# Optimization experiments

Hardware: AMD Instinct MI355X
Metric: run time of the kernel (lower is better)

The kernel has to match this reference:

```python
import jax, jax.numpy as jnp
import numpy as np

D_MODEL = 512
D_STATE = 16
D_CONV = 4
EXPAND = 2
D_INNER = EXPAND * D_MODEL          # 1024
DT_RANK = (D_MODEL + 15) // 16      # 32
B, L = 32, 2048
EPS = 1e-12


def _ln(x, g, b):
    mu = jnp.mean(x, axis=-1, keepdims=True)
    var = jnp.mean(jnp.square(x - mu), axis=-1, keepdims=True)
    return (x - mu) * jax.lax.rsqrt(var + EPS) * g + b


def setup_inputs() -> dict:
    key = jax.random.key(0)
    ks = jax.random.split(key, 12)
    s = lambda fan: 1.0 / np.sqrt(fan)
    inp = {
        "input_tensor": jax.random.normal(ks[0], (B, L, D_MODEL), jnp.float32),
        # Mamba params
        "in_proj_w": jax.random.normal(ks[1], (2 * D_INNER, D_MODEL), jnp.float32) * s(D_MODEL),
        "conv_w": jax.random.normal(ks[2], (D_INNER, D_CONV), jnp.float32) * s(D_CONV),
        "conv_b": jnp.zeros((D_INNER,), jnp.float32),
        "x_proj_w": jax.random.normal(ks[3], (DT_RANK + 2 * D_STATE, D_INNER), jnp.float32) * s(D_INNER),
        "dt_proj_w": jax.random.normal(ks[4], (D_INNER, DT_RANK), jnp.float32) * s(DT_RANK),
        "dt_proj_b": jnp.full((D_INNER,), -4.0, jnp.float32),  # softplus(-4) ~ small dt
        "A_log": jnp.log(jnp.broadcast_to(jnp.arange(1, D_STATE + 1, dtype=jnp.float32), (D_INNER, D_STATE))),
        "D": jnp.ones((D_INNER,), jnp.float32),
        "out_proj_w": jax.random.normal(ks[5], (D_MODEL, D_INNER), jnp.float32) * s(D_INNER),
        # block params
        "ln1_g": jnp.ones((D_MODEL,), jnp.float32),
        "ln1_b": jnp.zeros((D_MODEL,), jnp.float32),
        "w1_w": jax.random.normal(ks[6], (4 * D_MODEL, D_MODEL), jnp.float32) * s(D_MODEL),
        "w1_b": jnp.zeros((4 * D_MODEL,), jnp.float32),
        "w2_w": jax.random.normal(ks[7], (D_MODEL, 4 * D_MODEL), jnp.float32) * s(4 * D_MODEL),
        "w2_b": jnp.zeros((D_MODEL,), jnp.float32),
        "ln2_g": jnp.ones((D_MODEL,), jnp.float32),
        "ln2_b": jnp.zeros((D_MODEL,), jnp.float32),
    }
    return inp


def _mamba(x, in_proj_w, conv_w, conv_b, x_proj_w, dt_proj_w, dt_proj_b, A_log, D, out_proj_w):
    # x: [B, L, d_model]
    xz = jnp.einsum("bld,ed->ble", x, in_proj_w)          # [B,L,2*d_inner]
    xi, z = jnp.split(xz, 2, axis=-1)                      # each [B,L,d_inner]

    # depthwise causal conv1d along L (d_conv taps)
    xpad = jnp.pad(xi, ((0, 0), (D_CONV - 1, 0), (0, 0)))
    conv = conv_b
    for k in range(D_CONV):
        conv = conv + xpad[:, k:k + L, :] * conv_w[:, k]
    u = jax.nn.silu(conv)                                  # [B,L,d_inner]

    # input-dependent dt, B, C
    x_dbl = jnp.einsum("bld,ed->ble", u, x_proj_w)         # [B,L,dt_rank+2N]
    dt, B_t, C_t = jnp.split(x_dbl, [DT_RANK, DT_RANK + D_STATE], axis=-1)
    delta = jax.nn.softplus(jnp.einsum("blr,dr->bld", dt, dt_proj_w) + dt_proj_b)  # [B,L,d_inner]

    A = -jnp.exp(A_log)                                    # [d_inner, N]

    def step(h, inp):
        u_t, d_t, Bt, Ct = inp                             # [B,d_in],[B,d_in],[B,N],[B,N]
        dA = jnp.exp(d_t[..., None] * A)                   # [B,d_in,N]
        h = h * dA + (d_t * u_t)[..., None] * Bt[:, None, :]
        y = jnp.sum(h * Ct[:, None, :], axis=-1)           # [B,d_in]
        return h, y

    h0 = jnp.zeros((B, D_INNER, D_STATE), u.dtype)
    xs = (jnp.swapaxes(u, 0, 1), jnp.swapaxes(delta, 0, 1),
          jnp.swapaxes(B_t, 0, 1), jnp.swapaxes(C_t, 0, 1))
    _, ys = jax.lax.scan(step, h0, xs)                     # [L,B,d_inner]
    y = jnp.swapaxes(ys, 0, 1) + u * D
    y = y * jax.nn.silu(z)
    return jnp.einsum("ble,de->bld", y, out_proj_w)        # [B,L,d_model]


def reference(input_tensor, in_proj_w, conv_w, conv_b, x_proj_w, dt_proj_w, dt_proj_b,
              A_log, D, out_proj_w, ln1_g, ln1_b, w1_w, w1_b, w2_w, w2_b, ln2_g, ln2_b):
    h = _mamba(input_tensor, in_proj_w, conv_w, conv_b, x_proj_w, dt_proj_w,
               dt_proj_b, A_log, D, out_proj_w)
    h = _ln(h + input_tensor, ln1_g, ln1_b)                # num_layers > 1 branch, dropout=0
    f = jax.nn.gelu(jnp.einsum("bld,fd->blf", h, w1_w) + w1_b, approximate=False)
    f = jnp.einsum("blf,df->bld", f, w2_w) + w2_b
    return _ln(f + h, ln2_g, ln2_b)
```

## Files before the change

### kernel.cpp

```cpp
#include <hip/hip_runtime.h>
#include <hip/hip_bf16.h>

#define DM 512
#define DI 1024
#define DC 4
#define DTR 32
#define NST 16
#define LSEQ 2048
#define NBATCH 32
#define NCH 32
#define CHL 64

typedef __attribute__((ext_vector_type(8))) short b16x8;
typedef __attribute__((ext_vector_type(4))) float fx4;
typedef __attribute__((ext_vector_type(4))) unsigned short u16x4;

__device__ __forceinline__ unsigned short f2bf(float f) {
    union { float f; unsigned u; } x; x.f = f;
    unsigned r = x.u + 0x7fffu + ((x.u >> 16) & 1u);
    return (unsigned short)(r >> 16);
}
__device__ __forceinline__ float bf2f(unsigned short u) {
    union { unsigned u; float f; } x; x.u = ((unsigned)u) << 16;
    return x.f;
}

__global__ __launch_bounds__(256) void cast_kernel(const float* __restrict__ src,
                                                   unsigned short* __restrict__ dst, int n4) {
    int i = blockIdx.x * 256 + threadIdx.x;
    if (i < n4) {
        fx4 v = *(const fx4*)&src[(size_t)i * 4];
        u16x4 o;
        #pragma unroll
        for (int j = 0; j < 4; j++) o[j] = f2bf(v[j]);
        *(u16x4*)&dst[(size_t)i * 4] = o;
    }
}

template <int BN, int BK, int EPI, bool HAS_BIAS>
__global__ __launch_bounds__(256, 3) void gemm_bf16(const unsigned short* __restrict__ A,
                                                    const unsigned short* __restrict__ W,
                                                    const float* __restrict__ bias,
                                                    void* __restrict__ Cout, int N, int K,
                                                    unsigned short* __restrict__ aux) {
    constexpr int BM = 128;
    constexpr int GPR = BK / 8;
    __shared__ __align__(16) unsigned short As[BM * BK];
    __shared__ __align__(16) unsigned short Ws[BN * BK];
    const int tid = threadIdx.x;
    const int wave = tid >> 6, lane = tid & 63;
    const int lr = lane & 15, lg = lane >> 4;
    const int ntx = gridDim.x;
    const int tot = ntx * gridDim.y;
    const int lin = blockIdx.y * ntx + blockIdx.x;
    const int cpx = tot >> 3;
    const int swz = (lin & 7) * cpx + (lin >> 3);
    const int m0 = (swz / ntx) * BM, n0 = (swz % ntx) * BN;
    const int wm0 = (wave >> 1) * 64, wn0 = (wave & 1) * (BN / 2);
    constexpr int NR = BN / 32;
    fx4 acc[4][NR];
    #pragma unroll
    for (int i = 0; i < 4; i++)
        #pragma unroll
        for (int j = 0; j < NR; j++) acc[i][j] = fx4{0.f, 0.f, 0.f, 0.f};

    for (int k0 = 0; k0 < K; k0 += BK) {
        #pragma unroll
        for (int i = 0; i < (BM * BK / 8) / 256; i++) {
            int cb = (i * 4 + wave) * 64, c = cb + lane;
            int row = c / GPR, kk = (c % GPR) * 8;
            const unsigned short* g = A + (size_t)(m0 + row) * K + k0 + kk;
            __builtin_amdgcn_global_load_lds(
                (const __attribute__((address_space(1))) unsigned int*)g,
                (__attribute__((address_space(3))) unsigned int*)&As[cb * 8], 16, 0, 0);
        }
        #pragma unroll
        for (int i = 0; i < (BN * BK / 8) / 256; i++) {
            int cb = (i * 4 + wave) * 64, c = cb + lane;
            int row = c / GPR, kk = (c % GPR) * 8;
            const unsigned short* g = W + (size_t)(n0 + row) * K + k0 + kk;
            __builtin_amdgcn_global_load_lds(
                (const __attribute__((address_space(1))) unsigned int*)g,
                (__attribute__((address_space(3))) unsigned int*)&Ws[cb * 8], 16, 0, 0);
        }
        __syncthreads();
        #pragma unroll
        for (int ks = 0; ks < BK / 32; ks++) {
            b16x8 af[4], bfr[NR];
            #pragma unroll
            for (int mi = 0; mi < 4; mi++)
                af[mi] = *(const b16x8*)&As[(wm0 + mi * 16 + lr) * BK + ks * 32 + lg * 8];
            #pragma unroll
            for (int ni = 0; ni < NR; ni++)
                bfr[ni] = *(const b16x8*)&Ws[(wn0 + ni * 16 + lr) * BK + ks * 32 + lg * 8];
            #pragma unroll
            for (int mi = 0; mi < 4; mi++)
                #pragma unroll
                for (int ni = 0; ni < NR; ni++)
                    acc[mi][ni] = __builtin_amdgcn_mfma_f32_16x16x32_bf16(af[mi], bfr[ni],
                                                                         acc[mi][ni], 0, 0, 0);
        }
        __syncthreads();
    }
    #pragma unroll
    for (int mi = 0; mi < 4; mi++) {
        #pragma unroll
        for (int ni = 0; ni < NR; ni++) {
            #pragma unroll
            for (int j2 = 0; j2 < 4; j2++) {
                int row = m0 + wm0 + mi * 16 + lg * 4 + j2;
                int col = n0 + wn0 + ni * 16 + lr;
                float v = acc[mi][ni][j2];
                if (HAS_BIAS) v += bias[col];
                size_t o = (size_t)row * N + col;
                if (EPI == 0) {
                    ((float*)Cout)[o] = v;
                } else if (EPI == 1) {
                    ((unsigned short*)Cout)[o] = f2bf(v);
                } else if (EPI == 2) {
                    v = 0.5f * v * (1.f + erff(v * 0.70710678118654752f));
                    ((unsigned short*)Cout)[o] = f2bf(v);
                } else if (EPI == 3) {
                    v = (v > 20.f) ? v : log1pf(__expf(v));
                    ((float*)Cout)[o] = v;
                } else if (EPI == 4) {
                    v = (v > 20.f) ? v : log1pf(__expf(v));
                    ((unsigned short*)Cout)[o] = f2bf(v);
                } else {
                    ((float*)Cout)[o] = v;
                    if (col < DTR) aux[(size_t)row * DTR + col] = f2bf(v);
                }
            }
        }
    }
}

__global__ __launch_bounds__(256) void conv_silu_kernel(const unsigned short* __restrict__ xz16,
                                                        const float* __restrict__ cw,
                                                        const float* __restrict__ cb,
                                                        unsigned short* __restrict__ u16) {
    int idx = blockIdx.x * 256 + threadIdx.x;
    int strip = idx >> 7;
    int d0 = (idx & 127) << 3;
    int m0 = strip * 8;
    int l0 = m0 & (LSEQ - 1);
    fx4 w0[8];
    float bias[8];
    #pragma unroll
    for (int j = 0; j < 8; j++) {
        bias[j] = cb[d0 + j];
        w0[j] = *(const fx4*)&cw[(d0 + j) * 4];
    }
    float win[3][8];
    #pragma unroll
    for (int t = 0; t < 3; t++) {
        int lm = l0 - 3 + t;
        if (lm >= 0) {
            b16x8 xv = *(const b16x8*)&xz16[(size_t)(m0 - 3 + t) * (2 * DI) + d0];
            #pragma unroll
            for (int i = 0; i < 8; i++) win[t][i] = bf2f((unsigned short)xv[i]);
        } else {
            #pragma unroll
            for (int i = 0; i < 8; i++) win[t][i] = 0.f;
        }
    }
    #pragma unroll
    for (int j = 0; j < 8; j++) {
        float cur[8];
        b16x8 xv = *(const b16x8*)&xz16[(size_t)(m0 + j) * (2 * DI) + d0];
        #pragma unroll
        for (int i = 0; i < 8; i++) cur[i] = bf2f((unsigned short)xv[i]);
        b16x8 o;
        #pragma unroll
        for (int i = 0; i < 8; i++) {
            float v = bias[i] + win[0][i] * w0[i][0] + win[1][i] * w0[i][1] +
                      win[2][i] * w0[i][2] + cur[i] * w0[i][3];
            v = v / (1.f + __expf(-v));
            o[i] = (short)f2bf(v);
        }
        *(b16x8*)&u16[(size_t)(m0 + j) * DI + d0] = o;
        #pragma unroll
        for (int i = 0; i < 8; i++) {
            win[0][i] = win[1][i];
            win[1][i] = win[2][i];
            win[2][i] = cur[i];
        }
    }
}

__device__ __forceinline__ bool load_A(const float* __restrict__ A_log, int d, float* Av) {
    bool fast = true;
    #pragma unroll
    for (int n = 0; n < NST; n++) {
        Av[n] = -__expf(A_log[(size_t)d * NST + n]);
        fast = fast && (fabsf(Av[n] + (float)(n + 1)) < 1e-4f * (float)(n + 1));
    }
    return fast;
}

__device__ __forceinline__ void en_tree(float e1, float* en) {
    float e2 = e1 * e1, e3 = e2 * e1, e4 = e2 * e2, e8 = e4 * e4, e12 = e8 * e4;
    en[0] = e1;        en[1] = e2;        en[2] = e3;        en[3] = e4;
    en[4] = e4 * e1;   en[5] = e4 * e2;   en[6] = e4 * e3;   en[7] = e8;
    en[8] = e8 * e1;   en[9] = e8 * e2;   en[10] = e8 * e3;  en[11] = e12;
    en[12] = e12 * e1; en[13] = e12 * e2; en[14] = e12 * e3; en[15] = e8 * e8;
}

__global__ __launch_bounds__(256) void scan_partial(const unsigned short* __restrict__ delta16,
                                                    const unsigned short* __restrict__ u16,
                                                    const float* __restrict__ xdbl,
                                                    const float* __restrict__ A_log,
                                                    float* __restrict__ sumd,
                                                    float* __restrict__ hend) {
    int d = blockIdx.x * 256 + threadIdx.x;
    int ch = blockIdx.y, b = blockIdx.z;
    size_t bL = (size_t)b * LSEQ + (size_t)ch * CHL;
    float Av[NST], h[NST];
    const bool fast = load_A(A_log, d, Av);
    #pragma unroll
    for (int n = 0; n < NST; n++) h[n] = 0.f;
    float S = 0.f;
    #pragma unroll 2
    for (int l = 0; l < CHL; l++) {
        size_t r = bL + l;
        float dl = bf2f(delta16[r * DI + d]);
        float uu = bf2f(u16[r * DI + d]);
        S += dl;
        float du = dl * uu;
        const float* xr = &xdbl[r * 64 + 32];
        float Bv[NST];
        #pragma unroll
        for (int t = 0; t < 4; t++) *(fx4*)&Bv[t * 4] = *(const fx4*)(xr + t * 4);
        float en[NST];
        if (fast) {
            en_tree(__expf(-dl), en);
        } else {
            #pragma unroll
            for (int n = 0; n < NST; n++) en[n] = __expf(dl * Av[n]);
        }
        #pragma unroll
        for (int n = 0; n < NST; n++) h[n] = h[n] * en[n] + du * Bv[n];
    }
    size_t base = ((size_t)(b * NCH + ch) * NST) * DI + d;
    #pragma unroll
    for (int n = 0; n < NST; n++) hend[base + (size_t)n * DI] = h[n];
    sumd[(size_t)(b * NCH + ch) * DI + d] = S;
}

__global__ __launch_bounds__(256) void scan_carry(const float* __restrict__ sumd,
                                                  float* __restrict__ hend,
                                                  const float* __restrict__ A_log) {
    int d = blockIdx.x * 256 + threadIdx.x;
    int b = blockIdx.y;
    float Av[NST], h[NST];
    #pragma unroll
    for (int n = 0; n < NST; n++) {
        Av[n] = -__expf(A_log[(size_t)d * NST + n]);
        h[n] = 0.f;
    }
    for (int k = 0; k < NCH; k++) {
        size_t base = ((size_t)(b * NCH + k) * NST) * DI + d;
        if (k < NCH - 1) {
            float S = sumd[(size_t)(b * NCH + k) * DI + d];
            float he[NST];
            #pragma unroll
            for (int n = 0; n < NST; n++) he[n] = hend[base + (size_t)n * DI];
            #pragma unroll
            for (int n = 0; n < NST; n++) hend[base + (size_t)n * DI] = h[n];
            #pragma unroll
            for (int n = 0; n < NST; n++) h[n] = h[n] * __expf(S * Av[n]) + he[n];
        } else {
            #pragma unroll
            for (int n = 0; n < NST; n++) hend[base + (size_t)n * DI] = h[n];
        }
    }
}

__global__ __launch_bounds__(256) void scan_final(const unsigned short* __restrict__ delta16,
                                                  const unsigned short* u16,
                                                  const unsigned short* __restrict__ xz16,
                                                  const float* __restrict__ xdbl,
                                                  const float* __restrict__ A_log,
                                                  const float* __restrict__ Dp,
                                                  const float* __restrict__ hin,
                                                  unsigned short* y16) {
    int d = blockIdx.x * 256 + threadIdx.x;
    int ch = blockIdx.y, b = blockIdx.z;
    size_t bL = (size_t)b * LSEQ + (size_t)ch * CHL;
    float Av[NST], h[NST];
    const bool fast = load_A(A_log, d, Av);
    size_t base = ((size_t)(b * NCH + ch) * NST) * DI + d;
    #pragma unroll
    for (int n = 0; n < NST; n++) h[n] = hin[base + (size_t)n * DI];
    float Dd = Dp[d];
    #pragma unroll 2
    for (int l = 0; l < CHL; l++) {
        size_t r = bL + l;
        float dl = bf2f(delta16[r * DI + d]);
        float uu = bf2f(u16[r * DI + d]);
        float zz = bf2f(xz16[r * (2 * DI) + DI + d]);
        float du = dl * uu;
        const float* xr = &xdbl[r * 64 + 32];
        float Bv[NST], Cv[NST];
        #pragma unroll
        for (int t = 0; t < 4; t++) {
            *(fx4*)&Bv[t * 4] = *(const fx4*)(xr + t * 4);
            *(fx4*)&Cv[t * 4] = *(const fx4*)(xr + 16 + t * 4);
        }
        float en[NST];
        if (fast) {
            en_tree(__expf(-dl), en);
        } else {
            #pragma unroll
            for (int n = 0; n < NST; n++) en[n] = __expf(dl * Av[n]);
        }
        float y = 0.f;
        #pragma unroll
        for (int n = 0; n < NST; n++) {
            h[n] = h[n] * en[n] + du * Bv[n];
            y += h[n] * Cv[n];
        }
        y = (y + uu * Dd) * (zz / (1.f + __expf(-zz)));
        y16[r * DI + d] = f2bf(y);
    }
}

template <int AIN, int RIN, int OUT>
__global__ __launch_bounds__(256) void ln_kernel(const void* __restrict__ a,
                                                 const void* __restrict__ res,
                                                 const float* __restrict__ g,
                                                 const float* __restrict__ bta,
                                                 void* __restrict__ out) {
    int lane = threadIdx.x & 63;
    int row = blockIdx.x * 4 + (threadIdx.x >> 6);
    size_t base = (size_t)row * DM;
    int c0 = lane * 8;
    float av[8], rv[8];
    if (AIN == 0) {
        *(fx4*)&av[0] = *(const fx4*)&((const float*)a)[base + c0];
        *(fx4*)&av[4] = *(const fx4*)&((const float*)a)[base + c0 + 4];
    } else {
        b16x8 t = *(const b16x8*)&((const unsigned short*)a)[base + c0];
        #pragma unroll
        for (int i = 0; i < 8; i++) av[i] = bf2f((unsigned short)t[i]);
    }
    if (RIN == 0) {
        *(fx4*)&rv[0] = *(const fx4*)&((const float*)res)[base + c0];
        *(fx4*)&rv[4] = *(const fx4*)&((const float*)res)[base + c0 + 4];
    } else {
        b16x8 t = *(const b16x8*)&((const unsigned short*)res)[base + c0];
        #pragma unroll
        for (int i = 0; i < 8; i++) rv[i] = bf2f((unsigned short)t[i]);
    }
    float v[8], s = 0.f, q = 0.f;
    #pragma unroll
    for (int i = 0; i < 8; i++) {
        v[i] = av[i] + rv[i];
        s += v[i];
        q += v[i] * v[i];
    }
    #pragma unroll
    for (int m = 32; m >= 1; m >>= 1) {
        s += __shfl_xor(s, m);
        q += __shfl_xor(q, m);
    }
    float mu = s * (1.f / DM);
    float var = q * (1.f / DM) - mu * mu;
    float rsg = rsqrtf(var + 1e-12f);
    float gv[8], bv[8];
    *(fx4*)&gv[0] = *(const fx4*)&g[c0];
    *(fx4*)&gv[4] = *(const fx4*)&g[c0 + 4];
    *(fx4*)&bv[0] = *(const fx4*)&bta[c0];
    *(fx4*)&bv[4] = *(const fx4*)&bta[c0 + 4];
    if (OUT == 0) {
        fx4 o0, o1;
        #pragma unroll
        for (int i = 0; i < 4; i++) o0[i] = (v[i] - mu) * rsg * gv[i] + bv[i];
        #pragma unroll
        for (int i = 0; i < 4; i++) o1[i] = (v[4 + i] - mu) * rsg * gv[4 + i] + bv[4 + i];
        *(fx4*)&((float*)out)[base + c0] = o0;
        *(fx4*)&((float*)out)[base + c0 + 4] = o1;
    } else {
        b16x8 o;
        #pragma unroll
        for (int i = 0; i < 8; i++) o[i] = (short)f2bf((v[i] - mu) * rsg * gv[i] + bv[i]);
        *(b16x8*)&((unsigned short*)out)[base + c0] = o;
    }
}

static size_t align256(size_t b) { return (b + 255) & ~(size_t)255; }

static size_t tier_need(size_t Gb) {
    size_t R = Gb * LSEQ;
    size_t w = 0;
    w += align256((size_t)2 * DI * DM * 2);
    w += align256((size_t)64 * DI * 2);
    w += align256((size_t)DM * DI * 2);
    w += align256((size_t)4 * DM * DM * 2);
    w += align256((size_t)DM * 4 * DM * 2);
    w += align256((size_t)DI * DTR * 2);
    w += align256(R * 2048 * 2);
    w += align256(R * 1024 * 2);
    w += align256(R * 1024 * 2);
    w += align256(R * 64 * 4);
    w += align256(R * 32 * 2);
    w += align256(R * 512 * 2);
    w += align256(Gb * NCH * DI * 4);
    w += align256(Gb * NCH * NST * DI * 4);
    return w;
}

extern "C" void kernel_launch(void* const* d_in, const int* in_sizes, int n_in,
                              void* d_out, int out_size, void* d_ws, size_t ws_size,
                              hipStream_t stream) {
    const float* x_in   = (const float*)d_in[0];
    const float* inpw   = (const float*)d_in[1];
    const float* convw  = (const float*)d_in[2];
    const float* convb  = (const float*)d_in[3];
    const float* xprojw = (const float*)d_in[4];
    const float* dtw    = (const float*)d_in[5];
    const float* dtb    = (const float*)d_in[6];
    const float* A_log  = (const float*)d_in[7];
    const float* Dp     = (const float*)d_in[8];
    const float* outpw  = (const float*)d_in[9];
    const float* ln1g   = (const float*)d_in[10];
    const float* ln1b   = (const float*)d_in[11];
    const float* w1w    = (const float*)d_in[12];
    const float* w1b    = (const float*)d_in[13];
    const float* w2w    = (const float*)d_in[14];
    const float* w2b    = (const float*)d_in[15];
    const float* ln2g   = (const float*)d_in[16];
    const float* ln2b   = (const float*)d_in[17];

    int G = 1;
    const int tiers[5] = {32, 16, 8, 4, 2};
    for (int t = 0; t < 5; t++) {
        if (ws_size >= tier_need((size_t)tiers[t])) { G = tiers[t]; break; }
    }
    const size_t R = (size_t)G * LSEQ;

    char* w = (char*)d_ws;
    auto alloc = [&](size_t bytes) { char* p = w; w += align256(bytes); return p; };

    unsigned short* win16 = (unsigned short*)alloc((size_t)2 * DI * DM * 2);
    unsigned short* wxp16 = (unsigned short*)alloc((size_t)64 * DI * 2);
    unsigned short* wop16 = (unsigned short*)alloc((size_t)DM * DI * 2);
    unsigned short* ww116 = (unsigned short*)alloc((size_t)4 * DM * DM * 2);
    unsigned short* ww216 = (unsigned short*)alloc((size_t)DM * 4 * DM * 2);
    unsigned short* wdt16 = (unsigned short*)alloc((size_t)DI * DTR * 2);
    unsigned short* xz16  = (unsigned short*)alloc(R * 2048 * 2);
    unsigned short* u16   = (unsigned short*)alloc(R * 1024 * 2);
    unsigned short* dreg  = (unsigned short*)alloc(R * 1024 * 2);
    float*          xdbl  = (float*)alloc(R * 64 * 4);
    unsigned short* dt16  = (unsigned short*)alloc(R * 32 * 2);
    unsigned short* x16   = (unsigned short*)alloc(R * 512 * 2);
    float*          sumd  = (float*)alloc((size_t)G * NCH * DI * 4);
    float*          hend  = (float*)alloc((size_t)G * NCH * NST * DI * 4);

    unsigned short* delta16 = dreg;
    unsigned short* y16 = u16;
    unsigned short* f16 = xz16;
    unsigned short* mm16 = dreg;
    unsigned short* w2o16 = dreg;
    unsigned short* h16  = x16;

    dim3 blk(256);
    cast_kernel<<<(2 * DI * DM / 4 + 255) / 256, blk, 0, stream>>>(inpw, win16, 2 * DI * DM / 4);
    cast_kernel<<<(64 * DI / 4 + 255) / 256, blk, 0, stream>>>(xprojw, wxp16, 64 * DI / 4);
    cast_kernel<<<(DM * DI / 4 + 255) / 256, blk, 0, stream>>>(outpw, wop16, DM * DI / 4);
    cast_kernel<<<(4 * DM * DM / 4 + 255) / 256, blk, 0, stream>>>(w1w, ww116, 4 * DM * DM / 4);
    cast_kernel<<<(DM * 4 * DM / 4 + 255) / 256, blk, 0, stream>>>(w2w, ww216, DM * 4 * DM / 4);
    cast_kernel<<<(DI * DTR / 4 + 255) / 256, blk, 0, stream>>>(dtw, wdt16, DI * DTR / 4);

    for (int grp = 0; grp < NBATCH / G; grp++) {
        const size_t rb = (size_t)grp * R;
        const float* xg = x_in + rb * DM;
        cast_kernel<<<(int)(R * DM / 4 / 256), blk, 0, stream>>>(xg, x16, (int)(R * DM / 4));
        gemm_bf16<128, 64, 1, false><<<dim3(2 * DI / 128, R / 128), blk, 0, stream>>>(
            x16, win16, nullptr, xz16, 2 * DI, DM, nullptr);
        conv_silu_kernel<<<(int)(R / 16), blk, 0, stream>>>(xz16, convw, convb, u16);
        gemm_bf16<64, 64, 5, false><<<dim3(1, R / 128), blk, 0, stream>>>(
            u16, wxp16, nullptr, xdbl, 64, DI, dt16);
        gemm_bf16<128, 32, 4, true><<<dim3(DI / 128, R / 128), blk, 0, stream>>>(
            dt16, wdt16, dtb, delta16, DI, DTR, nullptr);
        scan_partial<<<dim3(DI / 256, NCH - 1, G), blk, 0, stream>>>(
            delta16, u16, xdbl, A_log, sumd, hend);
        scan_carry<<<dim3(DI / 256, G), blk, 0, stream>>>(sumd, hend, A_log);
        scan_final<<<dim3(DI / 256, NCH, G), blk, 0, stream>>>(
            delta16, u16, xz16, xdbl, A_log, Dp, hend, y16);
        gemm_bf16<128, 64, 1, false><<<dim3(DM / 128, R / 128), blk, 0, stream>>>(
            y16, wop16, nullptr, mm16, DM, DI, nullptr);
        ln_kernel<1, 0, 1><<<(int)(R / 4), blk, 0, stream>>>(mm16, xg, ln1g, ln1b, h16);
        gemm_bf16<128, 64, 2, true><<<dim3(4 * DM / 128, R / 128), blk, 0, stream>>>(
            h16, ww116, w1b, f16, 4 * DM, DM, nullptr);
        gemm_bf16<128, 64, 1, true><<<dim3(DM / 128, R / 128), blk, 0, stream>>>(
            f16, ww216, w2b, w2o16, DM, 4 * DM, nullptr);
        ln_kernel<1, 1, 0><<<(int)(R / 4), blk, 0, stream>>>(w2o16, h16, ln2g, ln2b,
                                                             (float*)d_out + rb * DM);
    }
}
```

Before: 1.639 ms.

## Double-buffer LDS tiles with XOR swizzle in BK=64 bf16 GEMM

For GEMM instantiations with BK=64, LDS is split into two A/W buffers so global-to-LDS loads for the next K tile are issued while MFMAs run on the current one. The LDS layout is XOR-swizzled on both the load and read side to reduce bank conflicts on the b16x8 fragment reads. Doubling LDS use lowers the occupancy hint from 3 to 2 blocks per CU, which trades latency hiding across blocks for overlap within a block. The loop assumes the number of K tiles is even.

Result: no change. 1.629 ms (-0.6%).

```diff
diff --git a/kernel.cpp b/kernel.cpp
--- a/kernel.cpp
+++ b/kernel.cpp
@@ -38,15 +38,16 @@
 }
 
 template <int BN, int BK, int EPI, bool HAS_BIAS>
-__global__ __launch_bounds__(256, 3) void gemm_bf16(const unsigned short* __restrict__ A,
+__global__ __launch_bounds__(256, 2) void gemm_bf16(const unsigned short* __restrict__ A,
                                                     const unsigned short* __restrict__ W,
                                                     const float* __restrict__ bias,
                                                     void* __restrict__ Cout, int N, int K,
                                                     unsigned short* __restrict__ aux) {
     constexpr int BM = 128;
-    constexpr int GPR = BK / 8;
-    __shared__ __align__(16) unsigned short As[BM * BK];
-    __shared__ __align__(16) unsigned short Ws[BN * BK];
+    constexpr int ASZ = BM * BK;
+    constexpr int WSZ = BN * BK;
+    constexpr int HALF = ASZ + WSZ;
+    __shared__ __align__(16) unsigned short lds[(BK == 64 ? 2 : 1) * HALF];
     const int tid = threadIdx.x;
     const int wave = tid >> 6, lane = tid & 63;
     const int lr = lane & 15, lg = lane >> 4;
@@ -64,44 +65,126 @@
         #pragma unroll
         for (int j = 0; j < NR; j++) acc[i][j] = fx4{0.f, 0.f, 0.f, 0.f};
 
-    for (int k0 = 0; k0 < K; k0 += BK) {
-        #pragma unroll
-        for (int i = 0; i < (BM * BK / 8) / 256; i++) {
-            int cb = (i * 4 + wave) * 64, c = cb + lane;
-            int row = c / GPR, kk = (c % GPR) * 8;
-            const unsigned short* g = A + (size_t)(m0 + row) * K + k0 + kk;
-            __builtin_amdgcn_global_load_lds(
-                (const __attribute__((address_space(1))) unsigned int*)g,
-                (__attribute__((address_space(3))) unsigned int*)&As[cb * 8], 16, 0, 0);
-        }
-        #pragma unroll
-        for (int i = 0; i < (BN * BK / 8) / 256; i++) {
-            int cb = (i * 4 + wave) * 64, c = cb + lane;
-            int row = c / GPR, kk = (c % GPR) * 8;
-            const unsigned short* g = W + (size_t)(n0 + row) * K + k0 + kk;
-            __builtin_amdgcn_global_load_lds(
-                (const __attribute__((address_space(1))) unsigned int*)g,
-                (__attribute__((address_space(3))) unsigned int*)&Ws[cb * 8], 16, 0, 0);
-        }
+    if constexpr (BK == 64) {
+#define VMCNT0 asm volatile("s_waitcnt vmcnt(0)" ::: "memory")
+#define STAGE(BUF, KT)                                                                   \
+    do {                                                                                 \
+        const int k0s = (KT) * 64;                                                       \
+        _Pragma("unroll")                                                                \
+        for (int i = 0; i < (BM * 64 / 8) / 256; i++) {                                  \
+            int ob = (i * 4 + wave) * 1024;                                              \
+            int o = ob + lane * 16;                                                      \
+            int s = o ^ (((o >> 7) & 3) << 5);                                           \
+            int row = s >> 7, cbyte = s & 127;                                           \
+            const unsigned short* g = A + (size_t)(m0 + row) * K + k0s + (cbyte >> 1);   \
+            __builtin_amdgcn_global_load_lds(                                            \
+                (const __attribute__((address_space(1))) unsigned int*)g,                \
+                (__attribute__((address_space(3))) unsigned int*)&lds[(BUF) * HALF +     \
+                                                                      (ob >> 1)],       \
+                16, 0, 0);                                                               \
+        }                                                                                \
+        _Pragma("unroll")                                                                \
+        for (int i = 0; i < (BN * 64 / 8) / 256; i++) {                                  \
+            int ob = (i * 4 + wave) * 1024;                                              \
+            int o = ob + lane * 16;                                                      \
+            int s = o ^ (((o >> 7) & 3) << 5);                                           \
+            int row = s >> 7, cbyte = s & 127;                                           \
+            const unsigned short* g = W + (size_t)(n0 + row) * K + k0s + (cbyte >> 1);   \
+            __builtin_amdgcn_global_load_lds(                                            \
+                (const __attribute__((address_space(1))) unsigned int*)g,                \
+                (__attribute__((address_space(3))) unsigned int*)&lds[(BUF) * HALF +     \
+                                                                      ASZ + (ob >> 1)], \
+                16, 0, 0);                                                               \
+        }                                                                                \
+    } while (0)
+#define COMPUTE(BUF)                                                                     \
+    do {                                                                                 \
+        _Pragma("unroll")                                                                \
+        for (int ks = 0; ks < 2; ks++) {                                                 \
+            b16x8 af[4], bfr[NR];                                                        \
+            _Pragma("unroll")                                                            \
+            for (int mi = 0; mi < 4; mi++) {                                             \
+                int ar = wm0 + mi * 16 + lr;                                             \
+                int ab = (ar * 64 + ks * 32 + lg * 8) * 2;                               \
+                ab ^= (ar & 3) << 5;                                                     \
+                af[mi] = *(const b16x8*)&lds[(BUF) * HALF + (ab >> 1)];                  \
+            }                                                                            \
+            _Pragma("unroll")                                                            \
+            for (int ni = 0; ni < NR; ni++) {                                            \
+                int wr = wn0 + ni * 16 + lr;                                             \
+                int wb = (wr * 64 + ks * 32 + lg * 8) * 2;                               \
+                wb ^= (wr & 3) << 5;                                                     \
+                bfr[ni] = *(const b16x8*)&lds[(BUF) * HALF + ASZ + (wb >> 1)];           \
+            }                                                                            \
+            _Pragma("unroll")                                                            \
+            for (int mi = 0; mi < 4; mi++)                                               \
+                _Pragma("unroll")                                                        \
+                for (int ni = 0; ni < NR; ni++)                                          \
+                    acc[mi][ni] = __builtin_amdgcn_mfma_f32_16x16x32_bf16(               \
+                        af[mi], bfr[ni], acc[mi][ni], 0, 0, 0);                          \
+        }                                                                                \
+    } while (0)
+        const int NT = K >> 6;
+        STAGE(0, 0);
+        VMCNT0;
         __syncthreads();
-        #pragma unroll
-        for (int ks = 0; ks < BK / 32; ks++) {
-            b16x8 af[4], bfr[NR];
-            #pragma unroll
-            for (int mi = 0; mi < 4; mi++)
-                af[mi] = *(const b16x8*)&As[(wm0 + mi * 16 + lr) * BK + ks * 32 + lg * 8];
-            #pragma unroll
-            for (int ni = 0; ni < NR; ni++)
-                bfr[ni] = *(const b16x8*)&Ws[(wn0 + ni * 16 + lr) * BK + ks * 32 + lg * 8];
-            #pragma unroll
-            for (int mi = 0; mi < 4; mi++)
+        for (int t = 0; t < NT; t += 2) {
+            STAGE(1, t + 1);
+            COMPUTE(0);
+            VMCNT0;
+            __syncthreads();
+            if (t + 2 < NT) STAGE(0, t + 2);
+            COMPUTE(1);
+            VMCNT0;
+            __syncthreads();
+        }
+#undef STAGE
+#undef COMPUTE
+#undef VMCNT0
+    } else {
+        unsigned short* As = lds;
+        unsigned short* Ws = lds + ASZ;
+        constexpr int GPR = BK / 8;
+        for (int k0 = 0; k0 < K; k0 += BK) {
+            #pragma unroll
+            for (int i = 0; i < (BM * BK / 8) / 256; i++) {
+                int cb = (i * 4 + wave) * 64, c = cb + lane;
+                int row = c / GPR, kk = (c % GPR) * 8;
+                const unsigned short* g = A + (size_t)(m0 + row) * K + k0 + kk;
+                __builtin_amdgcn_global_load_lds(
+                    (const __attribute__((address_space(1))) unsigned int*)g,
+                    (__attribute__((address_space(3))) unsigned int*)&As[cb * 8], 16, 0, 0);
+            }
+            #pragma unroll
+            for (int i = 0; i < (BN * BK / 8) / 256; i++) {
+                int cb = (i * 4 + wave) * 64, c = cb + lane;
+                int row = c / GPR, kk = (c % GPR) * 8;
+                const unsigned short* g = W + (size_t)(n0 + row) * K + k0 + kk;
+                __builtin_amdgcn_global_load_lds(
+                    (const __attribute__((address_space(1))) unsigned int*)g,
+                    (__attribute__((address_space(3))) unsigned int*)&Ws[cb * 8], 16, 0, 0);
+            }
+            __syncthreads();
+            #pragma unroll
+            for (int ks = 0; ks < BK / 32; ks++) {
+                b16x8 af[4], bfr[NR];
+                #pragma unroll
+                for (int mi = 0; mi < 4; mi++)
+                    af[mi] = *(const b16x8*)&As[(wm0 + mi * 16 + lr) * BK + ks * 32 + lg * 8];
                 #pragma unroll
                 for (int ni = 0; ni < NR; ni++)
-                    acc[mi][ni] = __builtin_amdgcn_mfma_f32_16x16x32_bf16(af[mi], bfr[ni],
-                                                                         acc[mi][ni], 0, 0, 0);
-        }
-        __syncthreads();
-    }
+                    bfr[ni] = *(const b16x8*)&Ws[(wn0 + ni * 16 + lr) * BK + ks * 32 + lg * 8];
+                #pragma unroll
+                for (int mi = 0; mi < 4; mi++)
+                    #pragma unroll
+                    for (int ni = 0; ni < NR; ni++)
+                        acc[mi][ni] = __builtin_amdgcn_mfma_f32_16x16x32_bf16(
+                            af[mi], bfr[ni], acc[mi][ni], 0, 0, 0);
+            }
+            __syncthreads();
+        }
+    }
+
     #pragma unroll
     for (int mi = 0; mi < 4; mi++) {
         #pragma unroll
```
